# Optimization experiments

Hardware: AMD Instinct MI355X
Metric: run time of the kernel (lower is better)

## Reference

```python
import jax, jax.numpy as jnp
import numpy as np

N = 100_000      # nodes
E = 1_600_000    # edges (avg degree 16)
D = 64           # node feature dim
C = 2            # num_classes
K = 2            # propagation hops


def setup_inputs() -> dict:
    key = jax.random.key(0)
    k1, k2, k3 = jax.random.split(key, 3)
    x = jax.random.normal(k1, (N, D), dtype=jnp.float32)
    edge_index = jax.random.randint(k2, (2, E), 0, N, dtype=jnp.int64)
    W = jax.random.normal(k3, (C, D), dtype=jnp.float32) * 0.1  # torch Linear weight [out,in]
    b = jnp.zeros((C,), dtype=jnp.float32)
    return {"x": x, "edge_index": edge_index, "W": W, "b": b}


def reference(x, edge_index, W, b):
    n = x.shape[0]
    self_loop = jnp.arange(n, dtype=edge_index.dtype)
    row = jnp.concatenate([edge_index[0], self_loop])  # source
    col = jnp.concatenate([edge_index[1], self_loop])  # target
    # GCN symmetric normalization with self-loops (PyG gcn_norm)
    deg = jax.ops.segment_sum(jnp.ones(col.shape, dtype=x.dtype), col, num_segments=n)
    dinv = jnp.where(deg > 0, jax.lax.rsqrt(deg), 0.0)
    norm = dinv[row] * dinv[col]                      # [E+N]
    # K-hop propagation: x <- A_hat x
    for _ in range(K):
        x = jax.ops.segment_sum(norm[:, None] * x[row], col, num_segments=n)
    logits = x @ W.T + b                               # [N, C]
    return jax.nn.log_softmax(logits, axis=1)
```

## Files before the change

### kernel.cpp

```cpp
#include <hip/hip_runtime.h>
#include <hip/hip_bf16.h>
#include <math.h>


#define NODES 100000
#define EDGES 1600000
#define DIM 64

#define PBITS 12
#define PSIZE 4096
#define P_BUCKETS 25
#define CAP 131072
#define NSLICE 10
#define PART_BLOCKS 256
#define SEG (EDGES / PART_BLOCKS)
#define PAIRS (SEG / 2)

__global__ void init_kernel(const void* ei, int* mode, int* cursor) {
  int t = threadIdx.x;
  const int* p = (const int*)ei;
  unsigned long long ball = __ballot(p[2 * t + 1] == 0);
  if (t == 0) *mode = (ball == ~0ULL) ? 1 : 0;
  if (t < P_BUCKETS) cursor[t] = t * CAP;
}

__global__ void partition_kernel(const void* ei, const int* __restrict__ mode,
                                 int* __restrict__ cursor,
                                 int2* __restrict__ ecbuf) {
  __shared__ int lcnt[P_BUCKETS];
  __shared__ int lbase[P_BUCKETS];
  int t = threadIdx.x;
  int m = *mode;
  int pbase = blockIdx.x * PAIRS;

  if (t < P_BUCKETS) lcnt[t] = 0;
  __syncthreads();

  if (m) {
    const longlong2* cp =
        (const longlong2*)((const long long*)ei + EDGES) + pbase;
    for (int i = t; i < PAIRS; i += 256) {
      longlong2 v = cp[i];
      atomicAdd(&lcnt[((int)v.x) >> PBITS], 1);
      atomicAdd(&lcnt[((int)v.y) >> PBITS], 1);
    }
  } else {
    const int2* cp = (const int2*)((const int*)ei + EDGES) + pbase;
    for (int i = t; i < PAIRS; i += 256) {
      int2 v = cp[i];
      atomicAdd(&lcnt[v.x >> PBITS], 1);
      atomicAdd(&lcnt[v.y >> PBITS], 1);
    }
  }
  __syncthreads();
  if (t < P_BUCKETS) {
    lbase[t] = atomicAdd(&cursor[t], lcnt[t]);
    lcnt[t] = 0;
  }
  __syncthreads();

  if (m) {
    const longlong2* rp = (const longlong2*)ei + pbase;
    const longlong2* cp =
        (const longlong2*)((const long long*)ei + EDGES) + pbase;
    for (int i = t; i < PAIRS; i += 256) {
      longlong2 rv = rp[i];
      longlong2 cv = cp[i];
      int r0 = (int)rv.x, c0 = (int)cv.x;
      int b0 = c0 >> PBITS;
      int p0 = lbase[b0] + atomicAdd(&lcnt[b0], 1);
      if (p0 < (b0 + 1) * CAP) ecbuf[p0] = make_int2(r0, c0 & (PSIZE - 1));
      int r1 = (int)rv.y, c1 = (int)cv.y;
      int b1 = c1 >> PBITS;
      int p1 = lbase[b1] + atomicAdd(&lcnt[b1], 1);
      if (p1 < (b1 + 1) * CAP) ecbuf[p1] = make_int2(r1, c1 & (PSIZE - 1));
    }
  } else {
    const int2* rp = (const int2*)ei + pbase;
    const int2* cp = (const int2*)((const int*)ei + EDGES) + pbase;
    for (int i = t; i < PAIRS; i += 256) {
      int2 rv = rp[i];
      int2 cv = cp[i];
      int b0 = cv.x >> PBITS;
      int p0 = lbase[b0] + atomicAdd(&lcnt[b0], 1);
      if (p0 < (b0 + 1) * CAP) ecbuf[p0] = make_int2(rv.x, cv.x & (PSIZE - 1));
      int b1 = cv.y >> PBITS;
      int p1 = lbase[b1] + atomicAdd(&lcnt[b1], 1);
      if (p1 < (b1 + 1) * CAP) ecbuf[p1] = make_int2(rv.y, cv.y & (PSIZE - 1));
    }
  }
}

__global__ void deg_kernel(const int* __restrict__ cursor,
                           const int2* __restrict__ ecbuf,
                           float* __restrict__ dinv) {
  __shared__ int h[PSIZE];
  int p = blockIdx.x;
  for (int i = threadIdx.x; i < PSIZE; i += 1024) h[i] = 0;
  __syncthreads();
  int base = p * CAP;
  int cnt = min(cursor[p] - base, CAP);
  for (int e = threadIdx.x; e < cnt; e += 1024)
    atomicAdd(&h[ecbuf[base + e].y], 1);
  __syncthreads();
  int gbase = p << PBITS;
  for (int i = threadIdx.x; i < PSIZE; i += 1024) {
    int g = gbase + i;
    if (g < NODES) dinv[g] = rsqrtf((float)(h[i] + 1));
  }
}

__global__ void proj_kernel(const float* __restrict__ x,
                            const float* __restrict__ W,
                            const float* __restrict__ dinv,
                            float2* __restrict__ ts) {
  int wid = (blockIdx.x * (blockDim.x >> 6)) + (threadIdx.x >> 6);
  int d = threadIdx.x & 63;
  if (wid >= NODES) return;
  float xv = x[(size_t)wid * DIM + d];
  float p0 = xv * W[d];
  float p1 = xv * W[DIM + d];
#pragma unroll
  for (int off = 32; off >= 1; off >>= 1) {
    p0 += __shfl_xor(p0, off, 64);
    p1 += __shfl_xor(p1, off, 64);
  }
  if (d == 0) {
    float di = dinv[wid];
    float2 t;
    t.x = di * p0;
    t.y = di * p1;
    ts[wid] = t;
  }
}

__global__ void hop_kernel(const int* __restrict__ cursor,
                           const int2* __restrict__ ecbuf,
                           const float2* __restrict__ feat,
                           float2* __restrict__ hpart) {
  __shared__ float lx[PSIZE];
  __shared__ float ly[PSIZE];
  int p = blockIdx.x / NSLICE, s = blockIdx.x % NSLICE;
  for (int i = threadIdx.x; i < PSIZE; i += 512) {
    lx[i] = 0.f;
    ly[i] = 0.f;
  }
  __syncthreads();
  int base = p * CAP;
  int cnt = min(cursor[p] - base, CAP);
  int per = (cnt + NSLICE - 1) / NSLICE;
  int beg = base + s * per;
  int end = min(base + cnt, beg + per);
  for (int e = beg + threadIdx.x; e < end; e += 512) {
    int2 ec = ecbuf[e];
    float2 v = feat[ec.x];
    atomicAdd(&lx[ec.y], v.x);
    atomicAdd(&ly[ec.y], v.y);
  }
  __syncthreads();
  float2* outp = hpart + (size_t)blockIdx.x * PSIZE;
  for (int i = threadIdx.x; i < PSIZE; i += 512) {
    float2 o;
    o.x = lx[i];
    o.y = ly[i];
    outp[i] = o;
  }
}

__global__ void merge1_kernel(const float2* __restrict__ hpart,
                              const float2* __restrict__ ts,
                              const float* __restrict__ dinv,
                              float2* __restrict__ z) {
  int i = blockIdx.x * blockDim.x + threadIdx.x;
  if (i >= NODES) return;
  int p = i >> PBITS, l = i & (PSIZE - 1);
  float2 t0 = ts[i];
  float ax = t0.x, ay = t0.y;
#pragma unroll
  for (int s = 0; s < NSLICE; s++) {
    float2 v = hpart[(size_t)(p * NSLICE + s) * PSIZE + l];
    ax += v.x;
    ay += v.y;
  }
  float di = dinv[i];
  float sc = di * di;
  float2 o;
  o.x = sc * ax;
  o.y = sc * ay;
  z[i] = o;
}

__global__ void merge2_kernel(const float2* __restrict__ hpart,
                              const float2* __restrict__ z,
                              const float* __restrict__ dinv,
                              const float* __restrict__ bias,
                              float2* __restrict__ out) {
  int i = blockIdx.x * blockDim.x + threadIdx.x;
  if (i >= NODES) return;
  int p = i >> PBITS, l = i & (PSIZE - 1);
  float2 z0 = z[i];
  float ax = z0.x, ay = z0.y;
#pragma unroll
  for (int s = 0; s < NSLICE; s++) {
    float2 v = hpart[(size_t)(p * NSLICE + s) * PSIZE + l];
    ax += v.x;
    ay += v.y;
  }
  float di = dinv[i];
  float l0 = di * ax + bias[0];
  float l1 = di * ay + bias[1];
  float m = fmaxf(l0, l1);
  float ls = m + logf(expf(l0 - m) + expf(l1 - m));
  float2 o;
  o.x = l0 - ls;
  o.y = l1 - ls;
  out[i] = o;
}

extern "C" void kernel_launch(void* const* d_in, const int* in_sizes, int n_in,
                              void* d_out, int out_size, void* d_ws,
                              size_t ws_size, hipStream_t stream) {
  const float* x = (const float*)d_in[0];
  const void* ei = d_in[1];
  const float* W = (const float*)d_in[2];
  const float* b = (const float*)d_in[3];
  float2* out = (float2*)d_out;

  char* w = (char*)d_ws;
  size_t off = 0;
  auto alloc = [&](size_t bytes) -> char* {
    char* p = w + off;
    off += (bytes + 255) & ~(size_t)255;
    return p;
  };
  int* mode = (int*)alloc(sizeof(int));
  int* cursor = (int*)alloc(P_BUCKETS * sizeof(int));
  int2* ecbuf = (int2*)alloc((size_t)P_BUCKETS * CAP * sizeof(int2));
  float* dinv = (float*)alloc(NODES * sizeof(float));
  float2* ts = (float2*)alloc(NODES * sizeof(float2));
  float2* z = (float2*)alloc(NODES * sizeof(float2));
  float2* hpart =
      (float2*)alloc((size_t)P_BUCKETS * NSLICE * PSIZE * sizeof(float2));
  (void)ws_size;

  const int NGRID = (NODES + 255) / 256;

  init_kernel<<<1, 64, 0, stream>>>(ei, mode, cursor);
  partition_kernel<<<PART_BLOCKS, 256, 0, stream>>>(ei, mode, cursor, ecbuf);
  deg_kernel<<<P_BUCKETS, 1024, 0, stream>>>(cursor, ecbuf, dinv);

  const int WPB = 256 / 64;
  proj_kernel<<<(NODES + WPB - 1) / WPB, 256, 0, stream>>>(x, W, dinv, ts);

  hop_kernel<<<P_BUCKETS * NSLICE, 512, 0, stream>>>(cursor, ecbuf, ts, hpart);
  merge1_kernel<<<NGRID, 256, 0, stream>>>(hpart, ts, dinv, z);
  hop_kernel<<<P_BUCKETS * NSLICE, 512, 0, stream>>>(cursor, ecbuf, z, hpart);
  merge2_kernel<<<NGRID, 256, 0, stream>>>(hpart, z, dinv, b, out);
}
```

Before: 177.4 us.

## Shrink buckets to 256 nodes, pack edges, fuse deg/proj and hop/merge kernels

Target buckets shrink from 4096 to 256 nodes, so each block owns a whole bucket. This removes the per-slice partial buffers and the separate merge kernels, with the merge folded into the hop kernels. Edges are packed into one int (source<<8 | local target), halving edge-buffer traffic. The degree histogram and projection are fused into one launch, and mode detection and cursor init are folded into the partition kernel plus a memset. Risks include overflow of the 8192 per-bucket capacity, unnormalized projection stored with dinv applied at gather time, and more global cursor atomics across 391 buckets.

Result: faster. 154.2 us (-13.1%).

```diff
diff --git a/kernel.cpp b/kernel.cpp
--- a/kernel.cpp
+++ b/kernel.cpp
@@ -7,55 +7,56 @@
 #define EDGES 1600000
 #define DIM 64
 
-#define PBITS 12
-#define PSIZE 4096
-#define P_BUCKETS 25
-#define CAP 131072
-#define NSLICE 10
+#define PBITS 8
+#define PSIZE 256
+#define P_BUCKETS 391
+#define CAP 8192
+
 #define PART_BLOCKS 256
-#define SEG (EDGES / PART_BLOCKS)
-#define PAIRS (SEG / 2)
-
-__global__ void init_kernel(const void* ei, int* mode, int* cursor) {
-  int t = threadIdx.x;
-  const int* p = (const int*)ei;
-  unsigned long long ball = __ballot(p[2 * t + 1] == 0);
-  if (t == 0) *mode = (ball == ~0ULL) ? 1 : 0;
-  if (t < P_BUCKETS) cursor[t] = t * CAP;
-}
-
-__global__ void partition_kernel(const void* ei, const int* __restrict__ mode,
-                                 int* __restrict__ cursor,
-                                 int2* __restrict__ ecbuf) {
+#define PART_EDGES (EDGES / PART_BLOCKS)
+#define PART_PAIRS (PART_EDGES / 2)
+
+#define PROJ_BLOCKS 782
+#define NODES_PER_PROJ 128
+
+__global__ __launch_bounds__(256) void part_kernel(const void* __restrict__ ei,
+                                                   int* __restrict__ cursor,
+                                                   int* __restrict__ ecbuf) {
+  __shared__ int shMode;
   __shared__ int lcnt[P_BUCKETS];
   __shared__ int lbase[P_BUCKETS];
-  int t = threadIdx.x;
-  int m = *mode;
-  int pbase = blockIdx.x * PAIRS;
-
-  if (t < P_BUCKETS) lcnt[t] = 0;
-  __syncthreads();
+  const int t = threadIdx.x;
+  if (t < 64) {
+    const int* p = (const int*)ei;
+    unsigned long long ball = __ballot(p[2 * t + 1] == 0);
+    if (t == 0) shMode = (ball == ~0ULL) ? 1 : 0;
+  }
+  for (int i = t; i < P_BUCKETS; i += 256) lcnt[i] = 0;
+  __syncthreads();
+  const int m = shMode;
+  const int pbase = blockIdx.x * PART_PAIRS;
 
   if (m) {
     const longlong2* cp =
         (const longlong2*)((const long long*)ei + EDGES) + pbase;
-    for (int i = t; i < PAIRS; i += 256) {
+    for (int i = t; i < PART_PAIRS; i += 256) {
       longlong2 v = cp[i];
       atomicAdd(&lcnt[((int)v.x) >> PBITS], 1);
       atomicAdd(&lcnt[((int)v.y) >> PBITS], 1);
     }
   } else {
     const int2* cp = (const int2*)((const int*)ei + EDGES) + pbase;
-    for (int i = t; i < PAIRS; i += 256) {
+    for (int i = t; i < PART_PAIRS; i += 256) {
       int2 v = cp[i];
       atomicAdd(&lcnt[v.x >> PBITS], 1);
       atomicAdd(&lcnt[v.y >> PBITS], 1);
     }
   }
   __syncthreads();
-  if (t < P_BUCKETS) {
-    lbase[t] = atomicAdd(&cursor[t], lcnt[t]);
-    lcnt[t] = 0;
+  for (int i = t; i < P_BUCKETS; i += 256) {
+    int c = lcnt[i];
+    lbase[i] = c ? atomicAdd(&cursor[i], c) : 0;
+    lcnt[i] = 0;
   }
   __syncthreads();
 
@@ -63,158 +64,141 @@
     const longlong2* rp = (const longlong2*)ei + pbase;
     const longlong2* cp =
         (const longlong2*)((const long long*)ei + EDGES) + pbase;
-    for (int i = t; i < PAIRS; i += 256) {
+    for (int i = t; i < PART_PAIRS; i += 256) {
       longlong2 rv = rp[i];
       longlong2 cv = cp[i];
-      int r0 = (int)rv.x, c0 = (int)cv.x;
-      int b0 = c0 >> PBITS;
-      int p0 = lbase[b0] + atomicAdd(&lcnt[b0], 1);
-      if (p0 < (b0 + 1) * CAP) ecbuf[p0] = make_int2(r0, c0 & (PSIZE - 1));
-      int r1 = (int)rv.y, c1 = (int)cv.y;
-      int b1 = c1 >> PBITS;
-      int p1 = lbase[b1] + atomicAdd(&lcnt[b1], 1);
-      if (p1 < (b1 + 1) * CAP) ecbuf[p1] = make_int2(r1, c1 & (PSIZE - 1));
+      {
+        int r = (int)rv.x, c = (int)cv.x, bk = c >> PBITS;
+        int rel = lbase[bk] + atomicAdd(&lcnt[bk], 1);
+        if (rel < CAP) ecbuf[bk * CAP + rel] = (r << PBITS) | (c & (PSIZE - 1));
+      }
+      {
+        int r = (int)rv.y, c = (int)cv.y, bk = c >> PBITS;
+        int rel = lbase[bk] + atomicAdd(&lcnt[bk], 1);
+        if (rel < CAP) ecbuf[bk * CAP + rel] = (r << PBITS) | (c & (PSIZE - 1));
+      }
     }
   } else {
     const int2* rp = (const int2*)ei + pbase;
     const int2* cp = (const int2*)((const int*)ei + EDGES) + pbase;
-    for (int i = t; i < PAIRS; i += 256) {
+    for (int i = t; i < PART_PAIRS; i += 256) {
       int2 rv = rp[i];
       int2 cv = cp[i];
-      int b0 = cv.x >> PBITS;
-      int p0 = lbase[b0] + atomicAdd(&lcnt[b0], 1);
-      if (p0 < (b0 + 1) * CAP) ecbuf[p0] = make_int2(rv.x, cv.x & (PSIZE - 1));
-      int b1 = cv.y >> PBITS;
-      int p1 = lbase[b1] + atomicAdd(&lcnt[b1], 1);
-      if (p1 < (b1 + 1) * CAP) ecbuf[p1] = make_int2(rv.y, cv.y & (PSIZE - 1));
-    }
-  }
-}
-
-__global__ void deg_kernel(const int* __restrict__ cursor,
-                           const int2* __restrict__ ecbuf,
-                           float* __restrict__ dinv) {
-  __shared__ int h[PSIZE];
-  int p = blockIdx.x;
-  for (int i = threadIdx.x; i < PSIZE; i += 1024) h[i] = 0;
-  __syncthreads();
-  int base = p * CAP;
-  int cnt = min(cursor[p] - base, CAP);
-  for (int e = threadIdx.x; e < cnt; e += 1024)
-    atomicAdd(&h[ecbuf[base + e].y], 1);
-  __syncthreads();
-  int gbase = p << PBITS;
-  for (int i = threadIdx.x; i < PSIZE; i += 1024) {
-    int g = gbase + i;
-    if (g < NODES) dinv[g] = rsqrtf((float)(h[i] + 1));
-  }
-}
-
-__global__ void proj_kernel(const float* __restrict__ x,
-                            const float* __restrict__ W,
-                            const float* __restrict__ dinv,
-                            float2* __restrict__ ts) {
-  int wid = (blockIdx.x * (blockDim.x >> 6)) + (threadIdx.x >> 6);
-  int d = threadIdx.x & 63;
-  if (wid >= NODES) return;
-  float xv = x[(size_t)wid * DIM + d];
-  float p0 = xv * W[d];
-  float p1 = xv * W[DIM + d];
+      {
+        int bk = cv.x >> PBITS;
+        int rel = lbase[bk] + atomicAdd(&lcnt[bk], 1);
+        if (rel < CAP)
+          ecbuf[bk * CAP + rel] = (rv.x << PBITS) | (cv.x & (PSIZE - 1));
+      }
+      {
+        int bk = cv.y >> PBITS;
+        int rel = lbase[bk] + atomicAdd(&lcnt[bk], 1);
+        if (rel < CAP)
+          ecbuf[bk * CAP + rel] = (rv.y << PBITS) | (cv.y & (PSIZE - 1));
+      }
+    }
+  }
+}
+
+__global__ __launch_bounds__(256) void degproj_kernel(
+    const int* __restrict__ cursor, const int* __restrict__ ecbuf,
+    const float* __restrict__ x, const float* __restrict__ W,
+    float4* __restrict__ uq) {
+  const int b = blockIdx.x;
+  const int t = threadIdx.x;
+  if (b < P_BUCKETS) {
+    __shared__ int h[PSIZE];
+    h[t] = 0;
+    __syncthreads();
+    const int cnt = min(cursor[b], CAP);
+    const int* ep = ecbuf + b * CAP;
+    for (int e = t; e < cnt; e += 256) atomicAdd(&h[ep[e] & (PSIZE - 1)], 1);
+    __syncthreads();
+    const int node = (b << PBITS) + t;
+    if (node < NODES) uq[node].z = rsqrtf((float)(h[t] + 1));
+  } else {
+    const int nbase = (b - P_BUCKETS) * NODES_PER_PROJ;
+    const int lane16 = t & 15;
+    const int sub = t >> 4;
+    const float4 w0 = *(const float4*)&W[lane16 * 4];
+    const float4 w1 = *(const float4*)&W[DIM + lane16 * 4];
+    for (int k = sub; k < NODES_PER_PROJ; k += 16) {
+      const int node = nbase + k;
+      if (node < NODES) {
+        float4 xv = *(const float4*)&x[(size_t)node * DIM + lane16 * 4];
+        float p0 = xv.x * w0.x + xv.y * w0.y + xv.z * w0.z + xv.w * w0.w;
+        float p1 = xv.x * w1.x + xv.y * w1.y + xv.z * w1.z + xv.w * w1.w;
 #pragma unroll
-  for (int off = 32; off >= 1; off >>= 1) {
-    p0 += __shfl_xor(p0, off, 64);
-    p1 += __shfl_xor(p1, off, 64);
-  }
-  if (d == 0) {
-    float di = dinv[wid];
-    float2 t;
-    t.x = di * p0;
-    t.y = di * p1;
-    ts[wid] = t;
-  }
-}
-
-__global__ void hop_kernel(const int* __restrict__ cursor,
-                           const int2* __restrict__ ecbuf,
-                           const float2* __restrict__ feat,
-                           float2* __restrict__ hpart) {
-  __shared__ float lx[PSIZE];
-  __shared__ float ly[PSIZE];
-  int p = blockIdx.x / NSLICE, s = blockIdx.x % NSLICE;
-  for (int i = threadIdx.x; i < PSIZE; i += 512) {
-    lx[i] = 0.f;
-    ly[i] = 0.f;
-  }
-  __syncthreads();
-  int base = p * CAP;
-  int cnt = min(cursor[p] - base, CAP);
-  int per = (cnt + NSLICE - 1) / NSLICE;
-  int beg = base + s * per;
-  int end = min(base + cnt, beg + per);
-  for (int e = beg + threadIdx.x; e < end; e += 512) {
-    int2 ec = ecbuf[e];
-    float2 v = feat[ec.x];
-    atomicAdd(&lx[ec.y], v.x);
-    atomicAdd(&ly[ec.y], v.y);
-  }
-  __syncthreads();
-  float2* outp = hpart + (size_t)blockIdx.x * PSIZE;
-  for (int i = threadIdx.x; i < PSIZE; i += 512) {
-    float2 o;
-    o.x = lx[i];
-    o.y = ly[i];
-    outp[i] = o;
-  }
-}
-
-__global__ void merge1_kernel(const float2* __restrict__ hpart,
-                              const float2* __restrict__ ts,
-                              const float* __restrict__ dinv,
-                              float2* __restrict__ z) {
-  int i = blockIdx.x * blockDim.x + threadIdx.x;
-  if (i >= NODES) return;
-  int p = i >> PBITS, l = i & (PSIZE - 1);
-  float2 t0 = ts[i];
-  float ax = t0.x, ay = t0.y;
-#pragma unroll
-  for (int s = 0; s < NSLICE; s++) {
-    float2 v = hpart[(size_t)(p * NSLICE + s) * PSIZE + l];
-    ax += v.x;
-    ay += v.y;
-  }
-  float di = dinv[i];
-  float sc = di * di;
-  float2 o;
-  o.x = sc * ax;
-  o.y = sc * ay;
-  z[i] = o;
-}
-
-__global__ void merge2_kernel(const float2* __restrict__ hpart,
-                              const float2* __restrict__ z,
-                              const float* __restrict__ dinv,
-                              const float* __restrict__ bias,
-                              float2* __restrict__ out) {
-  int i = blockIdx.x * blockDim.x + threadIdx.x;
-  if (i >= NODES) return;
-  int p = i >> PBITS, l = i & (PSIZE - 1);
-  float2 z0 = z[i];
-  float ax = z0.x, ay = z0.y;
-#pragma unroll
-  for (int s = 0; s < NSLICE; s++) {
-    float2 v = hpart[(size_t)(p * NSLICE + s) * PSIZE + l];
-    ax += v.x;
-    ay += v.y;
-  }
-  float di = dinv[i];
-  float l0 = di * ax + bias[0];
-  float l1 = di * ay + bias[1];
-  float m = fmaxf(l0, l1);
-  float ls = m + logf(expf(l0 - m) + expf(l1 - m));
-  float2 o;
-  o.x = l0 - ls;
-  o.y = l1 - ls;
-  out[i] = o;
+        for (int off = 8; off >= 1; off >>= 1) {
+          p0 += __shfl_xor(p0, off, 16);
+          p1 += __shfl_xor(p1, off, 16);
+        }
+        if (lane16 == 0) *(float2*)&uq[node] = make_float2(p0, p1);
+      }
+    }
+  }
+}
+
+__global__ __launch_bounds__(256) void hop1_kernel(
+    const int* __restrict__ cursor, const int* __restrict__ ecbuf,
+    const float4* __restrict__ uq, float2* __restrict__ z) {
+  __shared__ float ax[PSIZE];
+  __shared__ float ay[PSIZE];
+  const int b = blockIdx.x;
+  const int t = threadIdx.x;
+  ax[t] = 0.f;
+  ay[t] = 0.f;
+  __syncthreads();
+  const int cnt = min(cursor[b], CAP);
+  const int* ep = ecbuf + b * CAP;
+  for (int e = t; e < cnt; e += 256) {
+    int pk = ep[e];
+    float4 q = uq[pk >> PBITS];
+    int l = pk & (PSIZE - 1);
+    atomicAdd(&ax[l], q.z * q.x);
+    atomicAdd(&ay[l], q.z * q.y);
+  }
+  __syncthreads();
+  const int node = (b << PBITS) + t;
+  if (node < NODES) {
+    float4 q = uq[node];
+    float d = q.z;
+    float s = d * d;
+    z[node] = make_float2(s * (ax[t] + d * q.x), s * (ay[t] + d * q.y));
+  }
+}
+
+__global__ __launch_bounds__(256) void hop2_kernel(
+    const int* __restrict__ cursor, const int* __restrict__ ecbuf,
+    const float2* __restrict__ z, const float4* __restrict__ uq,
+    const float* __restrict__ bias, float2* __restrict__ out) {
+  __shared__ float ax[PSIZE];
+  __shared__ float ay[PSIZE];
+  const int b = blockIdx.x;
+  const int t = threadIdx.x;
+  ax[t] = 0.f;
+  ay[t] = 0.f;
+  __syncthreads();
+  const int cnt = min(cursor[b], CAP);
+  const int* ep = ecbuf + b * CAP;
+  for (int e = t; e < cnt; e += 256) {
+    int pk = ep[e];
+    float2 v = z[pk >> PBITS];
+    int l = pk & (PSIZE - 1);
+    atomicAdd(&ax[l], v.x);
+    atomicAdd(&ay[l], v.y);
+  }
+  __syncthreads();
+  const int node = (b << PBITS) + t;
+  if (node < NODES) {
+    float d = uq[node].z;
+    float2 zi = z[node];
+    float l0 = d * (ax[t] + zi.x) + bias[0];
+    float l1 = d * (ay[t] + zi.y) + bias[1];
+    float m = fmaxf(l0, l1);
+    float ls = m + logf(expf(l0 - m) + expf(l1 - m));
+    out[node] = make_float2(l0 - ls, l1 - ls);
+  }
 }
 
 extern "C" void kernel_launch(void* const* d_in, const int* in_sizes, int n_in,
@@ -223,7 +207,7 @@
   const float* x = (const float*)d_in[0];
   const void* ei = d_in[1];
   const float* W = (const float*)d_in[2];
-  const float* b = (const float*)d_in[3];
+  const float* bias = (const float*)d_in[3];
   float2* out = (float2*)d_out;
 
   char* w = (char*)d_ws;
@@ -233,27 +217,16 @@
     off += (bytes + 255) & ~(size_t)255;
     return p;
   };
-  int* mode = (int*)alloc(sizeof(int));
   int* cursor = (int*)alloc(P_BUCKETS * sizeof(int));
-  int2* ecbuf = (int2*)alloc((size_t)P_BUCKETS * CAP * sizeof(int2));
-  float* dinv = (float*)alloc(NODES * sizeof(float));
-  float2* ts = (float2*)alloc(NODES * sizeof(float2));
-  float2* z = (float2*)alloc(NODES * sizeof(float2));
-  float2* hpart =
-      (float2*)alloc((size_t)P_BUCKETS * NSLICE * PSIZE * sizeof(float2));
+  int* ecbuf = (int*)alloc((size_t)P_BUCKETS * CAP * sizeof(int));
+  float4* uq = (float4*)alloc((size_t)(P_BUCKETS << PBITS) * sizeof(float4));
+  float2* z = (float2*)alloc((size_t)NODES * sizeof(float2));
   (void)ws_size;
 
-  const int NGRID = (NODES + 255) / 256;
-
-  init_kernel<<<1, 64, 0, stream>>>(ei, mode, cursor);
-  partition_kernel<<<PART_BLOCKS, 256, 0, stream>>>(ei, mode, cursor, ecbuf);
-  deg_kernel<<<P_BUCKETS, 1024, 0, stream>>>(cursor, ecbuf, dinv);
-
-  const int WPB = 256 / 64;
-  proj_kernel<<<(NODES + WPB - 1) / WPB, 256, 0, stream>>>(x, W, dinv, ts);
-
-  hop_kernel<<<P_BUCKETS * NSLICE, 512, 0, stream>>>(cursor, ecbuf, ts, hpart);
-  merge1_kernel<<<NGRID, 256, 0, stream>>>(hpart, ts, dinv, z);
-  hop_kernel<<<P_BUCKETS * NSLICE, 512, 0, stream>>>(cursor, ecbuf, z, hpart);
-  merge2_kernel<<<NGRID, 256, 0, stream>>>(hpart, z, dinv, b, out);
-}
+  hipMemsetAsync(cursor, 0, P_BUCKETS * sizeof(int), stream);
+  part_kernel<<<PART_BLOCKS, 256, 0, stream>>>(ei, cursor, ecbuf);
+  degproj_kernel<<<P_BUCKETS + PROJ_BLOCKS, 256, 0, stream>>>(cursor, ecbuf, x,
+                                                              W, uq);
+  hop1_kernel<<<P_BUCKETS, 256, 0, stream>>>(cursor, ecbuf, uq, z);
+  hop2_kernel<<<P_BUCKETS, 256, 0, stream>>>(cursor, ecbuf, z, uq, bias, out);
+}
```
